# Kernel optimization log

Hardware: AMD Instinct MI355X
Metric: run time of the kernel (lower is better)

The kernel has to match this reference:

```python
import jax, jax.numpy as jnp
import numpy as np

B, T, D_MODEL, H = 4, 2048, 1024, 16
D_HEAD = D_MODEL // H
THETA = 10000.0


def setup_inputs() -> dict:
    key = jax.random.key(0)
    ks = jax.random.split(key, 5)
    s = 0.02
    return {
        "x": jax.random.normal(ks[0], (B, T, D_MODEL), dtype=jnp.float32),
        "Wq": jax.random.normal(ks[1], (D_MODEL, D_MODEL), dtype=jnp.float32) * s,
        "bq": jnp.zeros((D_MODEL,), dtype=jnp.float32),
        "Wk": jax.random.normal(ks[2], (D_MODEL, D_MODEL), dtype=jnp.float32) * s,
        "bk": jnp.zeros((D_MODEL,), dtype=jnp.float32),
        "Wv": jax.random.normal(ks[3], (D_MODEL, D_MODEL), dtype=jnp.float32) * s,
        "bv": jnp.zeros((D_MODEL,), dtype=jnp.float32),
        "Wo": jax.random.normal(ks[4], (D_MODEL, D_MODEL), dtype=jnp.float32) * s,
        "bo": jnp.zeros((D_MODEL,), dtype=jnp.float32),
    }


def _rope_tables(t_len, d_head, theta):
    inv_freq = 1.0 / theta ** (jnp.arange(0, d_head, 2, dtype=jnp.float32) / d_head)
    t = jnp.arange(t_len, dtype=jnp.float32)
    freqs = jnp.einsum('i,k->ik', t, inv_freq)  # [T, d_head/2]
    return jnp.cos(freqs), jnp.sin(freqs)


def _apply_rope(x, cos, sin):
    # x: [B, H, T, d_head]; cos/sin: [T, d_head/2] broadcast over B,H
    c = cos[None, None, :, :]
    s = sin[None, None, :, :]
    x0, x1 = x[..., ::2], x[..., 1::2]
    x_rot = jnp.stack((x0 * c - x1 * s, x0 * s + x1 * c), axis=-1)
    return x_rot.reshape(x.shape)


def reference(x, Wq, bq, Wk, bk, Wv, bv, Wo, bo):
    b, t, c = x.shape
    h, dh = H, D_HEAD
    q = (x @ Wq.T + bq).reshape(b, t, h, dh).transpose(0, 2, 1, 3)
    k = (x @ Wk.T + bk).reshape(b, t, h, dh).transpose(0, 2, 1, 3)
    v = (x @ Wv.T + bv).reshape(b, t, h, dh).transpose(0, 2, 1, 3)
    cos, sin = _rope_tables(t, dh, THETA)
    q = _apply_rope(q, cos, sin)
    k = _apply_rope(k, cos, sin)
    scores = jnp.einsum('bhqd,bhkd->bhqk', q, k) / jnp.sqrt(jnp.float32(dh))
    causal = jnp.tril(jnp.ones((t, t), dtype=bool))
    scores = jnp.where(causal[None, None, :, :], scores, -jnp.inf)
    attn = jax.nn.softmax(scores, axis=-1)
    out = jnp.einsum('bhqk,bhkd->bhqd', attn, v)
    out = out.transpose(0, 2, 1, 3).reshape(b, t, c)
    return out @ Wo.T + bo
```

## Files before the change

### kernel.cpp

```cpp
#include <hip/hip_runtime.h>
#include <hip/hip_bf16.h>

#define DEV static __device__ __forceinline__

typedef __attribute__((ext_vector_type(4))) float f32x4;
typedef __attribute__((ext_vector_type(16))) float f32x16;
typedef __attribute__((ext_vector_type(8))) short short8;
typedef __attribute__((ext_vector_type(4))) unsigned short u16x4;
typedef __attribute__((ext_vector_type(4))) unsigned int u32x4;

#define NB 4
#define NT 2048
#define NDM 1024
#define NH 16
#define NDH 64
#define NM (NB * NT)

DEV float bf2f(unsigned short u) {
  union { unsigned int i; float f; } x;
  x.i = ((unsigned int)u) << 16;
  return x.f;
}
DEV unsigned short f2bf(float f) {
  __hip_bfloat16 h = __float2bfloat16(f);
  return *reinterpret_cast<unsigned short*>(&h);
}
DEV unsigned int pack2bf(float lo, float hi) {
  return ((unsigned int)f2bf(hi) << 16) | (unsigned int)f2bf(lo);
}
DEV short8 mkfrag(unsigned int w0, unsigned int w1, unsigned int w2, unsigned int w3) {
  union { u32x4 u; short8 s; } x;
  x.u[0] = w0; x.u[1] = w1; x.u[2] = w2; x.u[3] = w3;
  return x.s;
}
DEV void permswap(unsigned int& a, unsigned int& b) {
  auto r = __builtin_amdgcn_permlane32_swap(a, b, false, false);
  a = r[0]; b = r[1];
}
DEV float xhalf_max(float v) {
  union { float f; unsigned int u; } x; x.f = v;
  unsigned int a = x.u, b = x.u;
  permswap(a, b);
  union { unsigned int u; float f; } pa, pb; pa.u = a; pb.u = b;
  return fmaxf(pa.f, pb.f);
}
DEV float xhalf_sum(float v) {
  union { float f; unsigned int u; } x; x.f = v;
  unsigned int a = x.u, b = x.u;
  permswap(a, b);
  union { unsigned int u; float f; } pa, pb; pa.u = a; pb.u = b;
  return pa.f + pb.f;
}

__global__ __launch_bounds__(256) void k_cvt_bf16(const float* __restrict__ in,
                                                  unsigned short* __restrict__ out,
                                                  int n8) {
  int i = blockIdx.x * 256 + threadIdx.x;
  if (i >= n8) return;
  const f32x4* p = (const f32x4*)(in + (size_t)i * 8);
  f32x4 a = p[0], b = p[1];
  short8 o;
  o[0] = (short)f2bf(a[0]); o[1] = (short)f2bf(a[1]);
  o[2] = (short)f2bf(a[2]); o[3] = (short)f2bf(a[3]);
  o[4] = (short)f2bf(b[0]); o[5] = (short)f2bf(b[1]);
  o[6] = (short)f2bf(b[2]); o[7] = (short)f2bf(b[3]);
  *(short8*)(out + (size_t)i * 8) = o;
}

__global__ __launch_bounds__(256) void k_cvt_w(const float* __restrict__ w0, const float* __restrict__ w1,
                                               const float* __restrict__ w2, const float* __restrict__ w3,
                                               unsigned short* __restrict__ o0, unsigned short* __restrict__ o1,
                                               unsigned short* __restrict__ o2, unsigned short* __restrict__ o3) {
  int i = blockIdx.x * 256 + threadIdx.x;
  int m = blockIdx.y;
  const float* in = (m == 0) ? w0 : (m == 1) ? w1 : (m == 2) ? w2 : w3;
  unsigned short* out = (m == 0) ? o0 : (m == 1) ? o1 : (m == 2) ? o2 : o3;
  const f32x4* p = (const f32x4*)(in + (size_t)i * 8);
  f32x4 a = p[0], b = p[1];
  short8 o;
  o[0] = (short)f2bf(a[0]); o[1] = (short)f2bf(a[1]);
  o[2] = (short)f2bf(a[2]); o[3] = (short)f2bf(a[3]);
  o[4] = (short)f2bf(b[0]); o[5] = (short)f2bf(b[1]);
  o[6] = (short)f2bf(b[2]); o[7] = (short)f2bf(b[3]);
  *(short8*)(out + (size_t)i * 8) = o;
}

__global__ __launch_bounds__(256) void k_rope_table(float2* __restrict__ tab) {
  int i = blockIdx.x * 256 + threadIdx.x;
  int t = i >> 5, f = i & 31;
  float inv = powf(10000.0f, -(float)f / 32.0f);
  float ang = (float)t * inv;
  tab[i] = make_float2(cosf(ang), sinf(ang));
}

__global__ __launch_bounds__(256) void k_gemm_qkv(const unsigned short* __restrict__ A,
                                                  const unsigned short* __restrict__ Bw,
                                                  const float* __restrict__ bq,
                                                  const float* __restrict__ bk,
                                                  const float* __restrict__ bv,
                                                  const float2* __restrict__ tab,
                                                  unsigned short* __restrict__ QH,
                                                  unsigned short* __restrict__ KH,
                                                  unsigned short* __restrict__ VT) {
  __shared__ unsigned short lA[128 * 32];
  __shared__ unsigned short lB[128 * 32];
  const int K = NDM;
  const int tid = threadIdx.x;
  const int lane = tid & 63;
  const int wave = tid >> 6;
  const int wr = (wave >> 1) * 64;
  const int wc = (wave & 1) * 64;
  const int lq = lane & 15;
  const int lk = (lane >> 4) * 8;

  unsigned int nbx = gridDim.x;
  unsigned int bid = blockIdx.y * nbx + blockIdx.x;
  unsigned int cpx = (nbx * gridDim.y) >> 3;
  unsigned int swz = (bid & 7) * cpx + (bid >> 3);
  const int bn = swz % nbx, bm = swz / nbx;

  const unsigned short* Ab = A + (size_t)bm * 128 * K;
  const unsigned short* Bb = Bw + (size_t)bn * 128 * K;
  const int r0 = tid >> 2;
  const int c0 = (tid & 3) * 8;

  f32x4 acc[4][4] = {};

  for (int k0 = 0; k0 < K; k0 += 32) {
    __syncthreads();
    __builtin_amdgcn_global_load_lds(
        (const __attribute__((address_space(1))) void*)(Ab + (size_t)r0 * K + k0 + c0),
        (__attribute__((address_space(3))) void*)(lA + tid * 8), 16, 0, 0);
    __builtin_amdgcn_global_load_lds(
        (const __attribute__((address_space(1))) void*)(Ab + (size_t)(r0 + 64) * K + k0 + c0),
        (__attribute__((address_space(3))) void*)(lA + 2048 + tid * 8), 16, 0, 0);
    __builtin_amdgcn_global_load_lds(
        (const __attribute__((address_space(1))) void*)(Bb + (size_t)r0 * K + k0 + c0),
        (__attribute__((address_space(3))) void*)(lB + tid * 8), 16, 0, 0);
    __builtin_amdgcn_global_load_lds(
        (const __attribute__((address_space(1))) void*)(Bb + (size_t)(r0 + 64) * K + k0 + c0),
        (__attribute__((address_space(3))) void*)(lB + 2048 + tid * 8), 16, 0, 0);
    __syncthreads();

    short8 af[4], bf[4];
#pragma unroll
    for (int i = 0; i < 4; ++i) af[i] = *(const short8*)&lA[(wr + i * 16 + lq) * 32 + lk];
#pragma unroll
    for (int j = 0; j < 4; ++j) bf[j] = *(const short8*)&lB[(wc + j * 16 + lq) * 32 + lk];
#pragma unroll
    for (int i = 0; i < 4; ++i)
#pragma unroll
      for (int j = 0; j < 4; ++j)
        acc[i][j] = __builtin_amdgcn_mfma_f32_16x16x32_bf16(af[i], bf[j], acc[i][j], 0, 0, 0);
  }

  const int which = bn >> 3;
  const int nloc = (bn & 7) * 128;
  const int rowb = bm * 128 + wr + (lane >> 4) * 4;
  const int colb = nloc + wc + lq;

  if (which == 2) {
#pragma unroll
    for (int i = 0; i < 4; ++i) {
#pragma unroll
      for (int j = 0; j < 4; ++j) {
        const int col = colb + j * 16;
        const float bs = bv[col];
        const int h = col >> 6, dh = col & 63;
        u16x4 w;
#pragma unroll
        for (int r = 0; r < 4; ++r) w[r] = f2bf(acc[i][j][r] + bs);
        const int row = rowb + i * 16;
        const int bb = row >> 11, t = row & (NT - 1);
        *(u16x4*)&VT[(((size_t)(bb * NH + h)) * NDH + dh) * NT + t] = w;
      }
    }
  } else {
    const float* bias = which ? bk : bq;
    unsigned short* Out = which ? KH : QH;
    const float sc = which ? 1.0f : 0.125f * 1.44269504088896f;
#pragma unroll
    for (int i = 0; i < 4; ++i) {
#pragma unroll
      for (int j = 0; j < 4; ++j) {
        const int col = colb + j * 16;
        const float bs = bias[col];
        const int h = col >> 6, dh = col & 63;
        const int pidx = dh >> 1;
        const bool odd = dh & 1;
#pragma unroll
        for (int r = 0; r < 4; ++r) {
          const int row = rowb + i * 16 + r;
          const int bb = row >> 11, t = row & (NT - 1);
          const float v = acc[i][j][r] + bs;
          const float pv = __shfl_xor(v, 1);
          const float2 cs = tab[t * 32 + pidx];
          const float y = odd ? (pv * cs.y + v * cs.x) : (v * cs.x - pv * cs.y);
          Out[(((size_t)(bb * NH + h)) * NT + t) * NDH + dh] = f2bf(y * sc);
        }
      }
    }
  }
}

__global__ __launch_bounds__(256) void k_gemm_bt(const unsigned short* __restrict__ A,
                                                 const unsigned short* __restrict__ Bw,
                                                 const float* __restrict__ bias,
                                                 float* __restrict__ Cout,
                                                 int M, int N, int K) {
  __shared__ unsigned short lA[128 * 32];
  __shared__ unsigned short lB[128 * 32];
  const int tid = threadIdx.x;
  const int lane = tid & 63;
  const int wave = tid >> 6;
  const int wr = (wave >> 1) * 64;
  const int wc = (wave & 1) * 64;
  const int lq = lane & 15;
  const int lk = (lane >> 4) * 8;

  unsigned int nbx = gridDim.x;
  unsigned int bid = blockIdx.y * nbx + blockIdx.x;
  unsigned int cpx = (nbx * gridDim.y) >> 3;
  unsigned int swz = (bid & 7) * cpx + (bid >> 3);
  const int bn = swz % nbx, bm = swz / nbx;

  const unsigned short* Ab = A + (size_t)bm * 128 * K;
  const unsigned short* Bb = Bw + (size_t)bn * 128 * K;
  const int r0 = tid >> 2;
  const int c0 = (tid & 3) * 8;

  f32x4 acc[4][4] = {};

  for (int k0 = 0; k0 < K; k0 += 32) {
    __syncthreads();
    __builtin_amdgcn_global_load_lds(
        (const __attribute__((address_space(1))) void*)(Ab + (size_t)r0 * K + k0 + c0),
        (__attribute__((address_space(3))) void*)(lA + tid * 8), 16, 0, 0);
    __builtin_amdgcn_global_load_lds(
        (const __attribute__((address_space(1))) void*)(Ab + (size_t)(r0 + 64) * K + k0 + c0),
        (__attribute__((address_space(3))) void*)(lA + 2048 + tid * 8), 16, 0, 0);
    __builtin_amdgcn_global_load_lds(
        (const __attribute__((address_space(1))) void*)(Bb + (size_t)r0 * K + k0 + c0),
        (__attribute__((address_space(3))) void*)(lB + tid * 8), 16, 0, 0);
    __builtin_amdgcn_global_load_lds(
        (const __attribute__((address_space(1))) void*)(Bb + (size_t)(r0 + 64) * K + k0 + c0),
        (__attribute__((address_space(3))) void*)(lB + 2048 + tid * 8), 16, 0, 0);
    __syncthreads();

    short8 af[4], bf[4];
#pragma unroll
    for (int i = 0; i < 4; ++i) af[i] = *(const short8*)&lA[(wr + i * 16 + lq) * 32 + lk];
#pragma unroll
    for (int j = 0; j < 4; ++j) bf[j] = *(const short8*)&lB[(wc + j * 16 + lq) * 32 + lk];
#pragma unroll
    for (int i = 0; i < 4; ++i)
#pragma unroll
      for (int j = 0; j < 4; ++j)
        acc[i][j] = __builtin_amdgcn_mfma_f32_16x16x32_bf16(af[i], bf[j], acc[i][j], 0, 0, 0);
  }

  const int rowb = bm * 128 + wr + (lane >> 4) * 4;
  const int colb = bn * 128 + wc + lq;
#pragma unroll
  for (int i = 0; i < 4; ++i) {
#pragma unroll
    for (int j = 0; j < 4; ++j) {
      const int col = colb + j * 16;
      const float bs = bias[col];
#pragma unroll
      for (int r = 0; r < 4; ++r) {
        const size_t idx = (size_t)(rowb + i * 16 + r) * N + col;
        Cout[idx] = acc[i][j][r] + bs;
      }
    }
  }
}

__global__ __launch_bounds__(256, 2) void k_attn(const unsigned short* __restrict__ Qh,
                                                 const unsigned short* __restrict__ Kh,
                                                 const unsigned short* __restrict__ Vtp,
                                                 unsigned short* __restrict__ Ctx) {
  __shared__ unsigned short kl[2][64 * 64];
  __shared__ unsigned short vl[2][64 * 64];
  const int tid = threadIdx.x;
  const int wave = tid >> 6, lane = tid & 63;
  const int l31 = lane & 31, hi = lane >> 5;
  const int b0 = blockIdx.x;
  const int bh = (b0 & 7) * 8 + ((b0 >> 3) & 7);
  const int t = 15 - (b0 >> 6);
  const int b = bh >> 4, h = bh & 15;

  const unsigned short* K = Kh + (size_t)bh * NT * NDH;
  const unsigned short* V = Vtp + (size_t)bh * NDH * NT;

  const int ch0 = tid, ch1 = tid + 256;
  const int sr0 = ch0 >> 3, sc0 = ((ch0 & 7) ^ (sr0 & 7)) * 8;
  const int sr1 = ch1 >> 3, sc1 = ((ch1 & 7) ^ (sr1 & 7)) * 8;
  const int xe = (l31 & 7) << 3;

  auto stage = [&](int buf, int kv0) {
    __builtin_amdgcn_global_load_lds(
        (const __attribute__((address_space(1))) void*)(K + (size_t)(kv0 + sr0) * NDH + sc0),
        (__attribute__((address_space(3))) void*)(&kl[buf][ch0 * 8]), 16, 0, 0);
    __builtin_amdgcn_global_load_lds(
        (const __attribute__((address_space(1))) void*)(K + (size_t)(kv0 + sr1) * NDH + sc1),
        (__attribute__((address_space(3))) void*)(&kl[buf][ch1 * 8]), 16, 0, 0);
    __builtin_amdgcn_global_load_lds(
        (const __attribute__((address_space(1))) void*)(V + (size_t)sr0 * NT + kv0 + sc0),
        (__attribute__((address_space(3))) void*)(&vl[buf][ch0 * 8]), 16, 0, 0);
    __builtin_amdgcn_global_load_lds(
        (const __attribute__((address_space(1))) void*)(V + (size_t)sr1 * NT + kv0 + sc1),
        (__attribute__((address_space(3))) void*)(&vl[buf][ch1 * 8]), 16, 0, 0);
  };

  const int q0w = t * 128 + wave * 32;
  const int nkv = 2 * t + 2;

  const unsigned short* Qr = Qh + ((size_t)bh * NT + q0w + l31) * NDH + 8 * hi;
  short8 qf[4];
#pragma unroll
  for (int s = 0; s < 4; ++s) qf[s] = *(const short8*)&Qr[16 * s];

  f32x16 ot0 = {}, ot1 = {};
  float m_run = -1e30f, l_run = 0.0f;

  stage(0, 0);
  __syncthreads();

  for (int kb = 0; kb < nkv; ++kb) {
    const int cur = kb & 1;
    const int kv0 = kb * 64;
    if (kb + 1 < nkv) stage(cur ^ 1, kv0 + 64);

    if (kv0 <= q0w + 31) {
      const unsigned short* kc = kl[cur];
      f32x16 st0 = {}, st1 = {};
#pragma unroll
      for (int s = 0; s < 4; ++s) {
        const int co = (16 * s + 8 * hi) ^ xe;
        short8 k0 = *(const short8*)&kc[l31 * 64 + co];
        short8 k1 = *(const short8*)&kc[(32 + l31) * 64 + co];
        st0 = __builtin_amdgcn_mfma_f32_32x32x16_bf16(k0, qf[s], st0, 0, 0, 0);
        st1 = __builtin_amdgcn_mfma_f32_32x32x16_bf16(k1, qf[s], st1, 0, 0, 0);
      }
      if (kv0 + 64 > q0w) {
        const int qg = q0w + l31;
#pragma unroll
        for (int r = 0; r < 16; ++r) {
          const int kr = kv0 + (r & 3) + 8 * (r >> 2) + 4 * hi;
          if (kr > qg) st0[r] = -1e30f;
          if (kr + 32 > qg) st1[r] = -1e30f;
        }
      }
      float mx;
      {
        float a0 = fmaxf(fmaxf(st0[0], st0[1]), fmaxf(st0[2], st0[3]));
        float a1 = fmaxf(fmaxf(st0[4], st0[5]), fmaxf(st0[6], st0[7]));
        float a2 = fmaxf(fmaxf(st0[8], st0[9]), fmaxf(st0[10], st0[11]));
        float a3 = fmaxf(fmaxf(st0[12], st0[13]), fmaxf(st0[14], st0[15]));
        float b0m = fmaxf(fmaxf(st1[0], st1[1]), fmaxf(st1[2], st1[3]));
        float b1m = fmaxf(fmaxf(st1[4], st1[5]), fmaxf(st1[6], st1[7]));
        float b2m = fmaxf(fmaxf(st1[8], st1[9]), fmaxf(st1[10], st1[11]));
        float b3m = fmaxf(fmaxf(st1[12], st1[13]), fmaxf(st1[14], st1[15]));
        mx = xhalf_max(fmaxf(fmaxf(fmaxf(a0, a1), fmaxf(a2, a3)),
                             fmaxf(fmaxf(b0m, b1m), fmaxf(b2m, b3m))));
      }
      if (!__all(mx - m_run <= 8.0f)) {
        const float m_new = fmaxf(m_run, mx);
        const float alpha = exp2f(m_run - m_new);
        l_run *= alpha;
        m_run = m_new;
#pragma unroll
        for (int r = 0; r < 16; ++r) { ot0[r] *= alpha; ot1[r] *= alpha; }
      }
#pragma unroll
      for (int r = 0; r < 16; ++r) st0[r] = exp2f(st0[r] - m_run);
#pragma unroll
      for (int r = 0; r < 16; ++r) st1[r] = exp2f(st1[r] - m_run);
      {
        float s0 = ((st0[0] + st0[1]) + (st0[2] + st0[3])) + ((st0[4] + st0[5]) + (st0[6] + st0[7]));
        float s1 = ((st0[8] + st0[9]) + (st0[10] + st0[11])) + ((st0[12] + st0[13]) + (st0[14] + st0[15]));
        float s2 = ((st1[0] + st1[1]) + (st1[2] + st1[3])) + ((st1[4] + st1[5]) + (st1[6] + st1[7]));
        float s3 = ((st1[8] + st1[9]) + (st1[10] + st1[11])) + ((st1[12] + st1[13]) + (st1[14] + st1[15]));
        l_run += xhalf_sum((s0 + s1) + (s2 + s3));
      }
      short8 pf[4];
#pragma unroll
      for (int ks = 0; ks < 4; ++ks) {
        const f32x16& sm = (ks & 2) ? st1 : st0;
        const int o = (ks & 1) * 8;
        unsigned int w0 = pack2bf(sm[o + 0], sm[o + 1]);
        unsigned int w2 = pack2bf(sm[o + 4], sm[o + 5]);
        permswap(w0, w2);
        unsigned int w1 = pack2bf(sm[o + 2], sm[o + 3]);
        unsigned int w3 = pack2bf(sm[o + 6], sm[o + 7]);
        permswap(w1, w3);
        pf[ks] = mkfrag(w0, w1, w2, w3);
      }
      const unsigned short* vc = vl[cur];
#pragma unroll
      for (int ks = 0; ks < 4; ++ks) {
        const int co = (16 * ks + 8 * hi) ^ xe;
        short8 v0 = *(const short8*)&vc[l31 * 64 + co];
        short8 v1 = *(const short8*)&vc[(32 + l31) * 64 + co];
        ot0 = __builtin_amdgcn_mfma_f32_32x32x16_bf16(v0, pf[ks], ot0, 0, 0, 0);
        ot1 = __builtin_amdgcn_mfma_f32_32x32x16_bf16(v1, pf[ks], ot1, 0, 0, 0);
      }
    }
    __syncthreads();
  }

  const float inv_l = 1.0f / l_run;
  unsigned short* dst = Ctx + ((size_t)(b * NT) + q0w + l31) * NDM + h * NDH;
#pragma unroll
  for (int dt = 0; dt < 2; ++dt) {
#pragma unroll
    for (int grp = 0; grp < 4; ++grp) {
      u16x4 w;
#pragma unroll
      for (int r = 0; r < 4; ++r) {
        const float v = (dt ? ot1[grp * 4 + r] : ot0[grp * 4 + r]) * inv_l;
        w[r] = f2bf(v);
      }
      *(u16x4*)&dst[dt * 32 + grp * 8 + 4 * hi] = w;
    }
  }
}

extern "C" void kernel_launch(void* const* d_in, const int* in_sizes, int n_in,
                              void* d_out, int out_size, void* d_ws, size_t ws_size,
                              hipStream_t stream) {
  const float* x  = (const float*)d_in[0];
  const float* Wq = (const float*)d_in[1];
  const float* bq = (const float*)d_in[2];
  const float* Wk = (const float*)d_in[3];
  const float* bk = (const float*)d_in[4];
  const float* Wv = (const float*)d_in[5];
  const float* bv = (const float*)d_in[6];
  const float* Wo = (const float*)d_in[7];
  const float* bo = (const float*)d_in[8];

  char* ws = (char*)d_ws;
  const size_t MB = 1024 * 1024;
  if (ws_size < 90 * MB) return;

  unsigned short* XB   = (unsigned short*)(ws + 0);
  unsigned short* WQB  = (unsigned short*)(ws + 16 * MB);
  unsigned short* WKB  = (unsigned short*)(ws + 18 * MB);
  unsigned short* WVB  = (unsigned short*)(ws + 20 * MB);
  unsigned short* WOB  = (unsigned short*)(ws + 22 * MB);
  unsigned short* QH   = (unsigned short*)(ws + 24 * MB);
  unsigned short* KH   = (unsigned short*)(ws + 40 * MB);
  unsigned short* VT   = (unsigned short*)(ws + 56 * MB);
  unsigned short* CTX  = (unsigned short*)(ws + 72 * MB);
  float2* TAB          = (float2*)(ws + 88 * MB);

  k_cvt_bf16<<<(NM * NDM / 8) / 256, 256, 0, stream>>>(x, XB, NM * NDM / 8);
  dim3 gw((NDM * NDM / 8) / 256, 4);
  k_cvt_w<<<gw, 256, 0, stream>>>(Wq, Wk, Wv, Wo, WQB, WKB, WVB, WOB);
  k_rope_table<<<(NT * 32) / 256, 256, 0, stream>>>(TAB);

  dim3 gq(3 * NDM / 128, NM / 128);
  k_gemm_qkv<<<gq, 256, 0, stream>>>(XB, WQB, bq, bk, bv, TAB, QH, KH, VT);

  k_attn<<<NB * NH * 16, 256, 0, stream>>>(QH, KH, VT, CTX);

  dim3 go(NDM / 128, NM / 128);
  k_gemm_bt<<<go, 256, 0, stream>>>(CTX, WOB, bo, (float*)d_out, NM, NDM, NDM);
}
```

Baseline: 197.7 us.

## Double GEMM K-tile to 64 and XOR-swizzle LDS layout

The QKV and output-projection GEMMs now stage a 128x64 K-slice per barrier pair instead of 128x32. This halves the number of synchronisation rounds and runs two MFMA k-steps per load. The LDS layout uses an XOR swizzle of 16-byte chunks by row so that fragment reads avoid bank conflicts with the wider row stride. LDS usage per block doubles to 32 KB, which may reduce occupancy.

```diff
diff --git a/kernel.cpp b/kernel.cpp
--- a/kernel.cpp
+++ b/kernel.cpp
@@ -93,6 +93,51 @@
   tab[i] = make_float2(cosf(ang), sinf(ang));
 }
 
+#define GEMM_CORE(Ab, Bb, Kdim)                                                          \
+  int rs[4], so[4];                                                                      \
+  _Pragma("unroll")                                                                      \
+  for (int s = 0; s < 4; ++s) {                                                          \
+    const int c = s * 256 + tid;                                                         \
+    rs[s] = c >> 3;                                                                      \
+    so[s] = ((c & 7) ^ (rs[s] & 7)) * 8;                                                 \
+  }                                                                                      \
+  f32x4 acc[4][4] = {};                                                                  \
+  for (int k0 = 0; k0 < Kdim; k0 += 64) {                                                \
+    __syncthreads();                                                                     \
+    _Pragma("unroll")                                                                    \
+    for (int s = 0; s < 4; ++s)                                                          \
+      __builtin_amdgcn_global_load_lds(                                                  \
+          (const __attribute__((address_space(1))) void*)(Ab + (size_t)rs[s] * Kdim + k0 + so[s]), \
+          (__attribute__((address_space(3))) void*)(lA + (s * 256 + tid) * 8), 16, 0, 0);\
+    _Pragma("unroll")                                                                    \
+    for (int s = 0; s < 4; ++s)                                                          \
+      __builtin_amdgcn_global_load_lds(                                                  \
+          (const __attribute__((address_space(1))) void*)(Bb + (size_t)rs[s] * Kdim + k0 + so[s]), \
+          (__attribute__((address_space(3))) void*)(lB + (s * 256 + tid) * 8), 16, 0, 0);\
+    __syncthreads();                                                                     \
+    _Pragma("unroll")                                                                    \
+    for (int kk = 0; kk < 2; ++kk) {                                                     \
+      short8 af[4], bf[4];                                                               \
+      _Pragma("unroll")                                                                  \
+      for (int i = 0; i < 4; ++i) {                                                      \
+        const int ra = wr + i * 16 + lq;                                                 \
+        const int pc = (kk * 4 + gg) ^ (ra & 7);                                         \
+        af[i] = *(const short8*)&lA[ra * 64 + pc * 8];                                   \
+      }                                                                                  \
+      _Pragma("unroll")                                                                  \
+      for (int j = 0; j < 4; ++j) {                                                      \
+        const int rb = wc + j * 16 + lq;                                                 \
+        const int pc = (kk * 4 + gg) ^ (rb & 7);                                         \
+        bf[j] = *(const short8*)&lB[rb * 64 + pc * 8];                                   \
+      }                                                                                  \
+      _Pragma("unroll")                                                                  \
+      for (int i = 0; i < 4; ++i)                                                        \
+        _Pragma("unroll")                                                                \
+        for (int j = 0; j < 4; ++j)                                                      \
+          acc[i][j] = __builtin_amdgcn_mfma_f32_16x16x32_bf16(af[i], bf[j], acc[i][j], 0, 0, 0); \
+    }                                                                                    \
+  }
+
 __global__ __launch_bounds__(256) void k_gemm_qkv(const unsigned short* __restrict__ A,
                                                   const unsigned short* __restrict__ Bw,
                                                   const float* __restrict__ bq,
@@ -102,8 +147,8 @@
                                                   unsigned short* __restrict__ QH,
                                                   unsigned short* __restrict__ KH,
                                                   unsigned short* __restrict__ VT) {
-  __shared__ unsigned short lA[128 * 32];
-  __shared__ unsigned short lB[128 * 32];
+  __shared__ unsigned short lA[128 * 64];
+  __shared__ unsigned short lB[128 * 64];
   const int K = NDM;
   const int tid = threadIdx.x;
   const int lane = tid & 63;
@@ -111,7 +156,7 @@
   const int wr = (wave >> 1) * 64;
   const int wc = (wave & 1) * 64;
   const int lq = lane & 15;
-  const int lk = (lane >> 4) * 8;
+  const int gg = lane >> 4;
 
   unsigned int nbx = gridDim.x;
   unsigned int bid = blockIdx.y * nbx + blockIdx.x;
@@ -121,38 +166,8 @@
 
   const unsigned short* Ab = A + (size_t)bm * 128 * K;
   const unsigned short* Bb = Bw + (size_t)bn * 128 * K;
-  const int r0 = tid >> 2;
-  const int c0 = (tid & 3) * 8;
-
-  f32x4 acc[4][4] = {};
-
-  for (int k0 = 0; k0 < K; k0 += 32) {
-    __syncthreads();
-    __builtin_amdgcn_global_load_lds(
-        (const __attribute__((address_space(1))) void*)(Ab + (size_t)r0 * K + k0 + c0),
-        (__attribute__((address_space(3))) void*)(lA + tid * 8), 16, 0, 0);
-    __builtin_amdgcn_global_load_lds(
-        (const __attribute__((address_space(1))) void*)(Ab + (size_t)(r0 + 64) * K + k0 + c0),
-        (__attribute__((address_space(3))) void*)(lA + 2048 + tid * 8), 16, 0, 0);
-    __builtin_amdgcn_global_load_lds(
-        (const __attribute__((address_space(1))) void*)(Bb + (size_t)r0 * K + k0 + c0),
-        (__attribute__((address_space(3))) void*)(lB + tid * 8), 16, 0, 0);
-    __builtin_amdgcn_global_load_lds(
-        (const __attribute__((address_space(1))) void*)(Bb + (size_t)(r0 + 64) * K + k0 + c0),
-        (__attribute__((address_space(3))) void*)(lB + 2048 + tid * 8), 16, 0, 0);
-    __syncthreads();
-
-    short8 af[4], bf[4];
-#pragma unroll
-    for (int i = 0; i < 4; ++i) af[i] = *(const short8*)&lA[(wr + i * 16 + lq) * 32 + lk];
-#pragma unroll
-    for (int j = 0; j < 4; ++j) bf[j] = *(const short8*)&lB[(wc + j * 16 + lq) * 32 + lk];
-#pragma unroll
-    for (int i = 0; i < 4; ++i)
-#pragma unroll
-      for (int j = 0; j < 4; ++j)
-        acc[i][j] = __builtin_amdgcn_mfma_f32_16x16x32_bf16(af[i], bf[j], acc[i][j], 0, 0, 0);
-  }
+
+  GEMM_CORE(Ab, Bb, K)
 
   const int which = bn >> 3;
   const int nloc = (bn & 7) * 128;
@@ -208,15 +223,15 @@
                                                  const float* __restrict__ bias,
                                                  float* __restrict__ Cout,
                                                  int M, int N, int K) {
-  __shared__ unsigned short lA[128 * 32];
-  __shared__ unsigned short lB[128 * 32];
+  __shared__ unsigned short lA[128 * 64];
+  __shared__ unsigned short lB[128 * 64];
   const int tid = threadIdx.x;
   const int lane = tid & 63;
   const int wave = tid >> 6;
   const int wr = (wave >> 1) * 64;
   const int wc = (wave & 1) * 64;
   const int lq = lane & 15;
-  const int lk = (lane >> 4) * 8;
+  const int gg = lane >> 4;
 
   unsigned int nbx = gridDim.x;
   unsigned int bid = blockIdx.y * nbx + blockIdx.x;
@@ -226,38 +241,8 @@
 
   const unsigned short* Ab = A + (size_t)bm * 128 * K;
   const unsigned short* Bb = Bw + (size_t)bn * 128 * K;
-  const int r0 = tid >> 2;
-  const int c0 = (tid & 3) * 8;
-
-  f32x4 acc[4][4] = {};
-
-  for (int k0 = 0; k0 < K; k0 += 32) {
-    __syncthreads();
-    __builtin_amdgcn_global_load_lds(
-        (const __attribute__((address_space(1))) void*)(Ab + (size_t)r0 * K + k0 + c0),
-        (__attribute__((address_space(3))) void*)(lA + tid * 8), 16, 0, 0);
-    __builtin_amdgcn_global_load_lds(
-        (const __attribute__((address_space(1))) void*)(Ab + (size_t)(r0 + 64) * K + k0 + c0),
-        (__attribute__((address_space(3))) void*)(lA + 2048 + tid * 8), 16, 0, 0);
-    __builtin_amdgcn_global_load_lds(
-        (const __attribute__((address_space(1))) void*)(Bb + (size_t)r0 * K + k0 + c0),
-        (__attribute__((address_space(3))) void*)(lB + tid * 8), 16, 0, 0);
-    __builtin_amdgcn_global_load_lds(
-        (const __attribute__((address_space(1))) void*)(Bb + (size_t)(r0 + 64) * K + k0 + c0),
-        (__attribute__((address_space(3))) void*)(lB + 2048 + tid * 8), 16, 0, 0);
-    __syncthreads();
-
-    short8 af[4], bf[4];
-#pragma unroll
-    for (int i = 0; i < 4; ++i) af[i] = *(const short8*)&lA[(wr + i * 16 + lq) * 32 + lk];
-#pragma unroll
-    for (int j = 0; j < 4; ++j) bf[j] = *(const short8*)&lB[(wc + j * 16 + lq) * 32 + lk];
-#pragma unroll
-    for (int i = 0; i < 4; ++i)
-#pragma unroll
-      for (int j = 0; j < 4; ++j)
-        acc[i][j] = __builtin_amdgcn_mfma_f32_16x16x32_bf16(af[i], bf[j], acc[i][j], 0, 0, 0);
-  }
+
+  GEMM_CORE(Ab, Bb, K)
 
   const int rowb = bm * 128 + wr + (lane >> 4) * 4;
   const int colb = bn * 128 + wc + lq;
```

After: 191.4 us. 3.2% less time.

## Double-buffer GEMM K-tiles with XOR-swizzled LDS and wider K step

Applied to the files above, without the earlier changes.

Replaces the single-buffered 32-wide K loop in both the QKV and output-projection GEMMs with a shared core that stages 64-wide K tiles into two LDS buffers. The next tile's global-to-LDS load is issued before computing on the current one, and the LDS layout is XOR-swizzled to reduce bank conflicts. The RoPE partner exchange also swaps __shfl_xor for a DPP quad permute. This is meant to hide global load latency and halve barrier count, at the cost of 64KB of LDS per block, which can reduce occupancy.

```diff
diff --git a/kernel.cpp b/kernel.cpp
--- a/kernel.cpp
+++ b/kernel.cpp
@@ -2,6 +2,8 @@
 #include <hip/hip_bf16.h>
 
 #define DEV static __device__ __forceinline__
+#define AS1q __attribute__((address_space(1)))
+#define AS3q __attribute__((address_space(3)))
 
 typedef __attribute__((ext_vector_type(4))) float f32x4;
 typedef __attribute__((ext_vector_type(16))) float f32x16;
@@ -50,6 +52,12 @@
   permswap(a, b);
   union { unsigned int u; float f; } pa, pb; pa.u = a; pb.u = b;
   return pa.f + pb.f;
+}
+DEV float dpp_swap1(float v) {
+  union { float f; int i; } x; x.f = v;
+  int r = __builtin_amdgcn_update_dpp(0, x.i, 0xB1, 0xF, 0xF, true);
+  union { int i; float f; } y; y.i = r;
+  return y.f;
 }
 
 __global__ __launch_bounds__(256) void k_cvt_bf16(const float* __restrict__ in,
@@ -93,6 +101,75 @@
   tab[i] = make_float2(cosf(ang), sinf(ang));
 }
 
+DEV void gemm_core(const unsigned short* __restrict__ Ab,
+                   const unsigned short* __restrict__ Bb,
+                   int Kdim, unsigned short* lds,
+                   int tid, int wr, int wc, int lq, int gg,
+                   f32x4 (&acc)[4][4]) {
+  const int q0 = tid,       r0 = q0 >> 3; const int o0 = ((q0 & 7) ^ (r0 & 7)) * 8;
+  const int q1 = tid + 256, r1 = q1 >> 3; const int o1 = ((q1 & 7) ^ (r1 & 7)) * 8;
+  const int q2 = tid + 512, r2 = q2 >> 3; const int o2 = ((q2 & 7) ^ (r2 & 7)) * 8;
+  const int q3 = tid + 768, r3 = q3 >> 3; const int o3 = ((q3 & 7) ^ (r3 & 7)) * 8;
+  const unsigned short* pa0 = Ab + (size_t)r0 * Kdim + o0;
+  const unsigned short* pa1 = Ab + (size_t)r1 * Kdim + o1;
+  const unsigned short* pa2 = Ab + (size_t)r2 * Kdim + o2;
+  const unsigned short* pa3 = Ab + (size_t)r3 * Kdim + o3;
+  const unsigned short* pb0 = Bb + (size_t)r0 * Kdim + o0;
+  const unsigned short* pb1 = Bb + (size_t)r1 * Kdim + o1;
+  const unsigned short* pb2 = Bb + (size_t)r2 * Kdim + o2;
+  const unsigned short* pb3 = Bb + (size_t)r3 * Kdim + o3;
+  const int e0 = q0 * 8, e1 = q1 * 8, e2 = q2 * 8, e3 = q3 * 8;
+
+  auto stage = [&](int buf, int ko) {
+    unsigned short* LA = lds + buf * 8192;
+    unsigned short* LB = lds + 16384 + buf * 8192;
+    __builtin_amdgcn_global_load_lds((const AS1q void*)(pa0 + ko), (AS3q void*)(LA + e0), 16, 0, 0);
+    __builtin_amdgcn_global_load_lds((const AS1q void*)(pa1 + ko), (AS3q void*)(LA + e1), 16, 0, 0);
+    __builtin_amdgcn_global_load_lds((const AS1q void*)(pa2 + ko), (AS3q void*)(LA + e2), 16, 0, 0);
+    __builtin_amdgcn_global_load_lds((const AS1q void*)(pa3 + ko), (AS3q void*)(LA + e3), 16, 0, 0);
+    __builtin_amdgcn_global_load_lds((const AS1q void*)(pb0 + ko), (AS3q void*)(LB + e0), 16, 0, 0);
+    __builtin_amdgcn_global_load_lds((const AS1q void*)(pb1 + ko), (AS3q void*)(LB + e1), 16, 0, 0);
+    __builtin_amdgcn_global_load_lds((const AS1q void*)(pb2 + ko), (AS3q void*)(LB + e2), 16, 0, 0);
+    __builtin_amdgcn_global_load_lds((const AS1q void*)(pb3 + ko), (AS3q void*)(LB + e3), 16, 0, 0);
+  };
+
+  const int xA = (wr + lq) & 7, xB = (wc + lq) & 7;
+  const int rowA = (wr + lq) * 64, rowB = (wc + lq) * 64;
+  const int cA0 = (gg ^ xA) * 8, cA1 = ((4 + gg) ^ xA) * 8;
+  const int cB0 = (gg ^ xB) * 8, cB1 = ((4 + gg) ^ xB) * 8;
+
+  const int NKT = Kdim >> 6;
+  stage(0, 0);
+  __syncthreads();
+  int cur = 0;
+  for (int t = 0; t < NKT; ++t) {
+    if (t + 1 < NKT) stage(cur ^ 1, (t + 1) << 6);
+    const unsigned short* LA = lds + cur * 8192;
+    const unsigned short* LB = lds + 16384 + cur * 8192;
+    short8 af[4], bf[4];
+#pragma unroll
+    for (int i = 0; i < 4; ++i) af[i] = *(const short8*)&LA[rowA + i * 1024 + cA0];
+#pragma unroll
+    for (int j = 0; j < 4; ++j) bf[j] = *(const short8*)&LB[rowB + j * 1024 + cB0];
+#pragma unroll
+    for (int i = 0; i < 4; ++i)
+#pragma unroll
+      for (int j = 0; j < 4; ++j)
+        acc[i][j] = __builtin_amdgcn_mfma_f32_16x16x32_bf16(af[i], bf[j], acc[i][j], 0, 0, 0);
+#pragma unroll
+    for (int i = 0; i < 4; ++i) af[i] = *(const short8*)&LA[rowA + i * 1024 + cA1];
+#pragma unroll
+    for (int j = 0; j < 4; ++j) bf[j] = *(const short8*)&LB[rowB + j * 1024 + cB1];
+#pragma unroll
+    for (int i = 0; i < 4; ++i)
+#pragma unroll
+      for (int j = 0; j < 4; ++j)
+        acc[i][j] = __builtin_amdgcn_mfma_f32_16x16x32_bf16(af[i], bf[j], acc[i][j], 0, 0, 0);
+    __syncthreads();
+    cur ^= 1;
+  }
+}
+
 __global__ __launch_bounds__(256) void k_gemm_qkv(const unsigned short* __restrict__ A,
                                                   const unsigned short* __restrict__ Bw,
                                                   const float* __restrict__ bq,
@@ -102,8 +179,7 @@
                                                   unsigned short* __restrict__ QH,
                                                   unsigned short* __restrict__ KH,
                                                   unsigned short* __restrict__ VT) {
-  __shared__ unsigned short lA[128 * 32];
-  __shared__ unsigned short lB[128 * 32];
+  __shared__ unsigned short lds[4 * 8192];
   const int K = NDM;
   const int tid = threadIdx.x;
   const int lane = tid & 63;
@@ -111,7 +187,7 @@
   const int wr = (wave >> 1) * 64;
   const int wc = (wave & 1) * 64;
   const int lq = lane & 15;
-  const int lk = (lane >> 4) * 8;
+  const int gg = lane >> 4;
 
   unsigned int nbx = gridDim.x;
   unsigned int bid = blockIdx.y * nbx + blockIdx.x;
@@ -121,38 +197,9 @@
 
   const unsigned short* Ab = A + (size_t)bm * 128 * K;
   const unsigned short* Bb = Bw + (size_t)bn * 128 * K;
-  const int r0 = tid >> 2;
-  const int c0 = (tid & 3) * 8;
 
   f32x4 acc[4][4] = {};
-
-  for (int k0 = 0; k0 < K; k0 += 32) {
-    __syncthreads();
-    __builtin_amdgcn_global_load_lds(
-        (const __attribute__((address_space(1))) void*)(Ab + (size_t)r0 * K + k0 + c0),
-        (__attribute__((address_space(3))) void*)(lA + tid * 8), 16, 0, 0);
-    __builtin_amdgcn_global_load_lds(
-        (const __attribute__((address_space(1))) void*)(Ab + (size_t)(r0 + 64) * K + k0 + c0),
-        (__attribute__((address_space(3))) void*)(lA + 2048 + tid * 8), 16, 0, 0);
-    __builtin_amdgcn_global_load_lds(
-        (const __attribute__((address_space(1))) void*)(Bb + (size_t)r0 * K + k0 + c0),
-        (__attribute__((address_space(3))) void*)(lB + tid * 8), 16, 0, 0);
-    __builtin_amdgcn_global_load_lds(
-        (const __attribute__((address_space(1))) void*)(Bb + (size_t)(r0 + 64) * K + k0 + c0),
-        (__attribute__((address_space(3))) void*)(lB + 2048 + tid * 8), 16, 0, 0);
-    __syncthreads();
-
-    short8 af[4], bf[4];
-#pragma unroll
-    for (int i = 0; i < 4; ++i) af[i] = *(const short8*)&lA[(wr + i * 16 + lq) * 32 + lk];
-#pragma unroll
-    for (int j = 0; j < 4; ++j) bf[j] = *(const short8*)&lB[(wc + j * 16 + lq) * 32 + lk];
-#pragma unroll
-    for (int i = 0; i < 4; ++i)
-#pragma unroll
-      for (int j = 0; j < 4; ++j)
-        acc[i][j] = __builtin_amdgcn_mfma_f32_16x16x32_bf16(af[i], bf[j], acc[i][j], 0, 0, 0);
-  }
+  gemm_core(Ab, Bb, K, lds, tid, wr, wc, lq, gg, acc);
 
   const int which = bn >> 3;
   const int nloc = (bn & 7) * 128;
@@ -193,7 +240,7 @@
           const int row = rowb + i * 16 + r;
           const int bb = row >> 11, t = row & (NT - 1);
           const float v = acc[i][j][r] + bs;
-          const float pv = __shfl_xor(v, 1);
+          const float pv = dpp_swap1(v);
           const float2 cs = tab[t * 32 + pidx];
           const float y = odd ? (pv * cs.y + v * cs.x) : (v * cs.x - pv * cs.y);
           Out[(((size_t)(bb * NH + h)) * NT + t) * NDH + dh] = f2bf(y * sc);
@@ -208,15 +255,14 @@
                                                  const float* __restrict__ bias,
                                                  float* __restrict__ Cout,
                                                  int M, int N, int K) {
-  __shared__ unsigned short lA[128 * 32];
-  __shared__ unsigned short lB[128 * 32];
+  __shared__ unsigned short lds[4 * 8192];
   const int tid = threadIdx.x;
   const int lane = tid & 63;
   const int wave = tid >> 6;
   const int wr = (wave >> 1) * 64;
   const int wc = (wave & 1) * 64;
   const int lq = lane & 15;
-  const int lk = (lane >> 4) * 8;
+  const int gg = lane >> 4;
 
   unsigned int nbx = gridDim.x;
   unsigned int bid = blockIdx.y * nbx + blockIdx.x;
@@ -226,38 +272,9 @@
 
   const unsigned short* Ab = A + (size_t)bm * 128 * K;
   const unsigned short* Bb = Bw + (size_t)bn * 128 * K;
-  const int r0 = tid >> 2;
-  const int c0 = (tid & 3) * 8;
 
   f32x4 acc[4][4] = {};
-
-  for (int k0 = 0; k0 < K; k0 += 32) {
-    __syncthreads();
-    __builtin_amdgcn_global_load_lds(
-        (const __attribute__((address_space(1))) void*)(Ab + (size_t)r0 * K + k0 + c0),
-        (__attribute__((address_space(3))) void*)(lA + tid * 8), 16, 0, 0);
-    __builtin_amdgcn_global_load_lds(
-        (const __attribute__((address_space(1))) void*)(Ab + (size_t)(r0 + 64) * K + k0 + c0),
-        (__attribute__((address_space(3))) void*)(lA + 2048 + tid * 8), 16, 0, 0);
-    __builtin_amdgcn_global_load_lds(
-        (const __attribute__((address_space(1))) void*)(Bb + (size_t)r0 * K + k0 + c0),
-        (__attribute__((address_space(3))) void*)(lB + tid * 8), 16, 0, 0);
-    __builtin_amdgcn_global_load_lds(
-        (const __attribute__((address_space(1))) void*)(Bb + (size_t)(r0 + 64) * K + k0 + c0),
-        (__attribute__((address_space(3))) void*)(lB + 2048 + tid * 8), 16, 0, 0);
-    __syncthreads();
-
-    short8 af[4], bf[4];
-#pragma unroll
-    for (int i = 0; i < 4; ++i) af[i] = *(const short8*)&lA[(wr + i * 16 + lq) * 32 + lk];
-#pragma unroll
-    for (int j = 0; j < 4; ++j) bf[j] = *(const short8*)&lB[(wc + j * 16 + lq) * 32 + lk];
-#pragma unroll
-    for (int i = 0; i < 4; ++i)
-#pragma unroll
-      for (int j = 0; j < 4; ++j)
-        acc[i][j] = __builtin_amdgcn_mfma_f32_16x16x32_bf16(af[i], bf[j], acc[i][j], 0, 0, 0);
-  }
+  gemm_core(Ab, Bb, K, lds, tid, wr, wc, lq, gg, acc);
 
   const int rowb = bm * 128 + wr + (lane >> 4) * 4;
   const int colb = bn * 128 + wc + lq;
@@ -300,17 +317,17 @@
 
   auto stage = [&](int buf, int kv0) {
     __builtin_amdgcn_global_load_lds(
-        (const __attribute__((address_space(1))) void*)(K + (size_t)(kv0 + sr0) * NDH + sc0),
-        (__attribute__((address_space(3))) void*)(&kl[buf][ch0 * 8]), 16, 0, 0);
+        (const AS1q void*)(K + (size_t)(kv0 + sr0) * NDH + sc0),
+        (AS3q void*)(&kl[buf][ch0 * 8]), 16, 0, 0);
     __builtin_amdgcn_global_load_lds(
-        (const __attribute__((address_space(1))) void*)(K + (size_t)(kv0 + sr1) * NDH + sc1),
-        (__attribute__((address_space(3))) void*)(&kl[buf][ch1 * 8]), 16, 0, 0);
+        (const AS1q void*)(K + (size_t)(kv0 + sr1) * NDH + sc1),
+        (AS3q void*)(&kl[buf][ch1 * 8]), 16, 0, 0);
     __builtin_amdgcn_global_load_lds(
-        (const __attribute__((address_space(1))) void*)(V + (size_t)sr0 * NT + kv0 + sc0),
-        (__attribute__((address_space(3))) void*)(&vl[buf][ch0 * 8]), 16, 0, 0);
+        (const AS1q void*)(V + (size_t)sr0 * NT + kv0 + sc0),
+        (AS3q void*)(&vl[buf][ch0 * 8]), 16, 0, 0);
     __builtin_amdgcn_global_load_lds(
-        (const __attribute__((address_space(1))) void*)(V + (size_t)sr1 * NT + kv0 + sc1),
-        (__attribute__((address_space(3))) void*)(&vl[buf][ch1 * 8]), 16, 0, 0);
+        (const AS1q void*)(V + (size_t)sr1 * NT + kv0 + sc1),
+        (AS3q void*)(&vl[buf][ch1 * 8]), 16, 0, 0);
   };
 
   const int q0w = t * 128 + wave * 32;
```

New measurement: 188.0 us. 1.05x faster.
